# Kernel optimization log

Measured on AMD Instinct MI355X. Metric: run time of the kernel, lower is better.

## Reference

```python
import jax, jax.numpy as jnp
import numpy as np

B, S, HID = 1, 2048, 2048
NH, NKV = 32, 8
HD = HID // NH  # 64
WINDOW = 1024
ROPE_BASE = 500000.0


def setup_inputs() -> dict:
    key = jax.random.key(0)
    ks = jax.random.split(key, 5)
    sc = 0.02
    return {
        "hidden_states": jax.random.normal(ks[0], (B, S, HID), dtype=jnp.float32),
        "Wq": jax.random.normal(ks[1], (HID, NH * HD), dtype=jnp.float32) * sc,
        "Wk": jax.random.normal(ks[2], (HID, NKV * HD), dtype=jnp.float32) * sc,
        "Wv": jax.random.normal(ks[3], (HID, NKV * HD), dtype=jnp.float32) * sc,
        "Wo": jax.random.normal(ks[4], (NH * HD, HID), dtype=jnp.float32) * sc,
    }


def _rope_cos_sin(seq_len, dtype):
    inv_freq = 1.0 / (ROPE_BASE ** (jnp.arange(0, HD, 2, dtype=jnp.float32) / HD))
    pos = jnp.arange(seq_len, dtype=jnp.float32)
    freqs = pos[:, None] * inv_freq[None, :]          # [S, HD/2]
    emb = jnp.concatenate([freqs, freqs], axis=-1)    # [S, HD]
    return jnp.cos(emb).astype(dtype), jnp.sin(emb).astype(dtype)


def _rotate_half(x):
    x1, x2 = x[..., : HD // 2], x[..., HD // 2:]
    return jnp.concatenate([-x2, x1], axis=-1)


def reference(hidden_states, Wq, Wk, Wv, Wo):
    b, s, _ = hidden_states.shape
    q = (hidden_states @ Wq).reshape(b, s, NH, HD).transpose(0, 2, 1, 3)   # [B,NH,S,D]
    k = (hidden_states @ Wk).reshape(b, s, NKV, HD).transpose(0, 2, 1, 3)  # [B,NKV,S,D]
    v = (hidden_states @ Wv).reshape(b, s, NKV, HD).transpose(0, 2, 1, 3)

    cos, sin = _rope_cos_sin(s, hidden_states.dtype)  # [S, D]
    cos, sin = cos[None, None], sin[None, None]       # [1,1,S,D]
    q = q * cos + _rotate_half(q) * sin
    k = k * cos + _rotate_half(k) * sin

    n_rep = NH // NKV
    k = jnp.repeat(k, n_rep, axis=1)  # [B,NH,S,D]
    v = jnp.repeat(v, n_rep, axis=1)

    # sliding-window causal additive mask
    row = jnp.arange(s)[:, None]
    col = jnp.arange(s)[None, :]
    banned = (col > row) | (col < row - WINDOW + 1)
    mask = jnp.where(banned, jnp.float32(-jnp.inf), 0.0).astype(hidden_states.dtype)

    scale = 1.0 / np.sqrt(HD)
    scores = jnp.einsum("bhqd,bhkd->bhqk", q, k) * scale + mask
    attn = jax.nn.softmax(scores, axis=-1)
    out = jnp.einsum("bhqk,bhkd->bhqd", attn, v)          # [B,NH,S,D]
    out = out.transpose(0, 2, 1, 3).reshape(b, s, NH * HD)
    return out @ Wo
```

## Files before the change

kernel.cpp:

```cpp
#include <hip/hip_runtime.h>
#include <hip/hip_bf16.h>
#include <math.h>

#define S_LEN 2048
#define HID 2048
#define NH 32
#define NKV 8
#define HD 64
#define WINDOW 1024
#define QBLK 128
#define QKVN 3072

typedef __attribute__((ext_vector_type(8))) short bx8;
typedef __attribute__((ext_vector_type(4))) float fx4;
typedef __attribute__((ext_vector_type(8))) unsigned short us8;

#define GL_LDS16(gp, lp) \
    __builtin_amdgcn_global_load_lds((__attribute__((address_space(1))) const void*)(gp), \
                                     (__attribute__((address_space(3))) void*)(lp), 16, 0, 0)

__global__ __launch_bounds__(256) void prep_kernel(const float* __restrict__ hs,
                                                   const float* __restrict__ Wq,
                                                   const float* __restrict__ Wk,
                                                   const float* __restrict__ Wv,
                                                   const float* __restrict__ Wo,
                                                   float* __restrict__ cosT, float* __restrict__ sinT,
                                                   __hip_bfloat16* __restrict__ hsb,
                                                   __hip_bfloat16* __restrict__ WqkvT,
                                                   __hip_bfloat16* __restrict__ WoT) {
    __shared__ float tile[32][33];
    int b = blockIdx.x, t = threadIdx.x;
    if (b < 256) {
        int idx = b * 256 + t;
        int s = idx >> 5, f = idx & 31;
        double inv = exp(-2.0 * (double)f / 64.0 * log(500000.0));
        double ang = (double)s * inv;
        cosT[idx] = (float)cos(ang);
        sinT[idx] = (float)sin(ang);
        return;
    }
    b -= 256;
    if (b < 2048) {
        int i = (b * 256 + t) * 8;
        float4 a = *reinterpret_cast<const float4*>(&hs[i]);
        float4 c = *reinterpret_cast<const float4*>(&hs[i + 4]);
        __hip_bfloat16 o[8] __attribute__((aligned(16)));
        o[0] = __float2bfloat16(a.x); o[1] = __float2bfloat16(a.y);
        o[2] = __float2bfloat16(a.z); o[3] = __float2bfloat16(a.w);
        o[4] = __float2bfloat16(c.x); o[5] = __float2bfloat16(c.y);
        o[6] = __float2bfloat16(c.z); o[7] = __float2bfloat16(c.w);
        *reinterpret_cast<bx8*>(&hsb[i]) = *reinterpret_cast<bx8*>(o);
        return;
    }
    b -= 2048;
    const float* src; __hip_bfloat16* dst; int Nd, bx, by;
    if (b < 4096)      { src = Wq; dst = WqkvT;                        Nd = 2048; bx = b & 63; by = b >> 6; }
    else if (b < 5120) { b -= 4096; src = Wk; dst = WqkvT + (size_t)2048 * 2048; Nd = 512; bx = b & 15; by = b >> 4; }
    else if (b < 6144) { b -= 5120; src = Wv; dst = WqkvT + (size_t)2560 * 2048; Nd = 512; bx = b & 15; by = b >> 4; }
    else               { b -= 6144; src = Wo; dst = WoT;               Nd = 2048; bx = b & 63; by = b >> 6; }
    int n0 = bx * 32, k0 = by * 32, tx = t & 31, ty = t >> 5;
#pragma unroll
    for (int i = 0; i < 4; i++)
        tile[ty + 8 * i][tx] = src[(size_t)(k0 + ty + 8 * i) * Nd + n0 + tx];
    __syncthreads();
#pragma unroll
    for (int i = 0; i < 4; i++)
        dst[(size_t)(n0 + ty + 8 * i) * 2048 + k0 + tx] = __float2bfloat16(tile[tx][ty + 8 * i]);
}

__global__ __launch_bounds__(256) void ropev_kernel(__hip_bfloat16* __restrict__ QKV,
                                                    __hip_bfloat16* __restrict__ Vt,
                                                    const float* __restrict__ cosT,
                                                    const float* __restrict__ sinT) {
    __shared__ __hip_bfloat16 tile[32][33];
    int b = blockIdx.x, t = threadIdx.x;
    if (b < 10240) {
        int idx = b * 256 + t;
        int f = idx & 31;
        int head = (idx >> 5) % (NH + NKV);
        int s = idx / ((NH + NKV) * 32);
        float c  = cosT[(s << 5) + f];
        float sn = sinT[(s << 5) + f];
        __hip_bfloat16* p = (head < NH) ? (QKV + (size_t)s * QKVN + head * HD)
                                        : (QKV + (size_t)s * QKVN + 2048 + (head - NH) * HD);
        float x1 = __bfloat162float(p[f]), x2 = __bfloat162float(p[f + 32]);
        p[f]      = __float2bfloat16(x1 * c - x2 * sn);
        p[f + 32] = __float2bfloat16(x2 * c + x1 * sn);
        return;
    }
    b -= 10240;
    int s0 = (b & 63) * 32, d0 = (b >> 6) * 32;
    int tx = t & 31, ty = t >> 5;
#pragma unroll
    for (int i = 0; i < 4; i++)
        tile[ty + 8 * i][tx] = QKV[(size_t)(s0 + ty + 8 * i) * QKVN + 2560 + d0 + tx];
    __syncthreads();
#pragma unroll
    for (int i = 0; i < 4; i++)
        Vt[(size_t)(d0 + ty + 8 * i) * S_LEN + s0 + tx] = tile[tx][ty + 8 * i];
}

template <int OUTBF16>
__global__ __launch_bounds__(256) void gemm_pipe_kernel(const __hip_bfloat16* __restrict__ A,
                                                        const __hip_bfloat16* __restrict__ Bt,
                                                        void* __restrict__ Cp,
                                                        int M, int N, int K, int stripe) {
    __shared__ __hip_bfloat16 As[3][2048];
    __shared__ __hip_bfloat16 Bs[3][4096];

    const int bid = blockIdx.x;
    const int x = bid & 7, j = bid >> 3;
    const int bn = (x * stripe + j % stripe) * 128;
    const int bm = (j / stripe) * 64;

    const int t = threadIdx.x, w = t >> 6, l = t & 63;
    const int wr = (w >> 1) * 32, wc = (w & 1) * 64;
    const int lr = l & 15;
    const int rdslot = (((l >> 4) ^ ((lr >> 1) & 3))) * 8;
    const int srow = w * 16 + (l >> 2);
    const int scol = (((l & 3) ^ ((l >> 3) & 3))) * 8;
    const int ldsoff = w * 512;

    const __hip_bfloat16* ga0 = A + (size_t)(bm + srow) * K + scol;
    const __hip_bfloat16* gb0 = Bt + (size_t)(bn + srow) * K + scol;
    const size_t half = (size_t)64 * K;

    fx4 acc[2][4];
#pragma unroll
    for (int m = 0; m < 2; m++)
#pragma unroll
        for (int n = 0; n < 4; n++) acc[m][n] = (fx4){0.f, 0.f, 0.f, 0.f};

    const int T = K >> 5;

#define STAGE(kt, b)                                              \
    do {                                                          \
        const __hip_bfloat16* ga = ga0 + (kt) * 32;               \
        const __hip_bfloat16* gb = gb0 + (kt) * 32;               \
        GL_LDS16(ga,        &As[(b)][ldsoff]);                    \
        GL_LDS16(gb,        &Bs[(b)][ldsoff]);                    \
        GL_LDS16(gb + half, &Bs[(b)][2048 + ldsoff]);             \
    } while (0)

    STAGE(0, 0);
    STAGE(1, 1);

    for (int i = 0; i < T; i++) {
        const int r = i % 3;
        if (i + 1 < T) asm volatile("s_waitcnt vmcnt(3)" ::: "memory");
        else           asm volatile("s_waitcnt vmcnt(0)" ::: "memory");
        __builtin_amdgcn_s_barrier();
        asm volatile("" ::: "memory");
        if (i + 2 < T) STAGE(i + 2, (i + 2) % 3);

        bx8 af[2], bf[4];
#pragma unroll
        for (int m = 0; m < 2; m++)
            af[m] = *reinterpret_cast<const bx8*>(&As[r][(wr + m * 16 + lr) * 32 + rdslot]);
#pragma unroll
        for (int n = 0; n < 4; n++)
            bf[n] = *reinterpret_cast<const bx8*>(&Bs[r][(wc + n * 16 + lr) * 32 + rdslot]);
#pragma unroll
        for (int m = 0; m < 2; m++)
#pragma unroll
            for (int n = 0; n < 4; n++)
                acc[m][n] = __builtin_amdgcn_mfma_f32_16x16x32_bf16(af[m], bf[n], acc[m][n], 0, 0, 0);
    }
#undef STAGE

    const int lq = (l >> 4) * 4;
#pragma unroll
    for (int m = 0; m < 2; m++)
#pragma unroll
        for (int n = 0; n < 4; n++)
#pragma unroll
            for (int r2 = 0; r2 < 4; r2++) {
                int row = bm + wr + m * 16 + lq + r2;
                int col = bn + wc + n * 16 + lr;
                float v = acc[m][n][r2];
                if (OUTBF16)
                    ((__hip_bfloat16*)Cp)[(size_t)row * N + col] = __float2bfloat16(v);
                else
                    ((float*)Cp)[(size_t)row * N + col] = v;
            }
}

__global__ __launch_bounds__(512, 4) void attn_kernel(const __hip_bfloat16* __restrict__ Q,
                                                      const __hip_bfloat16* __restrict__ Kg,
                                                      const __hip_bfloat16* __restrict__ Vtg,
                                                      __hip_bfloat16* __restrict__ Ab) {
    __shared__ __hip_bfloat16 Ks[64 * 64];
    __shared__ __hip_bfloat16 Vs[64 * 64];
    __shared__ __hip_bfloat16 Ps[QBLK * 64];

    const int bid = blockIdx.x;
    const int swz = (bid & 7) * 64 + (bid >> 3);
    const int h = swz >> 4, qi = swz & 15;
    const int qb = qi * QBLK;
    const int kvh = h >> 2;

    const int t = threadIdx.x, w = t >> 6, l = t & 63;
    const int lr = l & 15, g = l >> 4, lk = g * 8;
    const int qbw = qb + 16 * w;
    const int prow = 16 * w + lr;
    const int psz = (prow & 7) << 4;

    char* KsB = (char*)Ks;
    char* VsB = (char*)Vs;
    char* PsB = (char*)Ps;

    bx8 qa[2];
#pragma unroll
    for (int ks = 0; ks < 2; ks++)
        qa[ks] = *reinterpret_cast<const bx8*>(
            &Q[(size_t)(qbw + lr) * QKVN + h * HD + ks * 32 + lk]);

    fx4 ot[4];
#pragma unroll
    for (int n = 0; n < 4; n++) ot[n] = (fx4){0.f, 0.f, 0.f, 0.f};
    float mrow = -1e30f, srow = 0.f;

    const int k0_first = (qb >= 1024) ? (qb - 1024) : 0;
    const int k0_last  = qb + 64;
    const int wmax = qbw + 15;
    const int rowq = qbw + lr;

    const int sr = t >> 3, sc8 = (t & 7) * 8;
    const int dst = sr * 128 + ((sc8 * 2) ^ ((sr & 7) << 4));

    for (int k0 = k0_first; k0 <= k0_last; k0 += 64) {
        us8 kv = *reinterpret_cast<const us8*>(&Kg[(size_t)(k0 + sr) * QKVN + kvh * HD + sc8]);
        us8 vv = *reinterpret_cast<const us8*>(&Vtg[(size_t)(kvh * HD + sr) * S_LEN + k0 + sc8]);
        *reinterpret_cast<us8*>(KsB + dst) = kv;
        *reinterpret_cast<us8*>(VsB + dst) = vv;
        __syncthreads();

        if (k0 <= wmax) {
            bx8 kb[4][2];
#pragma unroll
            for (int n = 0; n < 4; n++)
#pragma unroll
                for (int ks = 0; ks < 2; ks++) {
                    int row = 16 * n + lr;
                    kb[n][ks] = *reinterpret_cast<const bx8*>(
                        KsB + row * 128 + (((ks * 64) + 16 * g) ^ ((row & 7) << 4)));
                }
            fx4 sc[4];
#pragma unroll
            for (int n = 0; n < 4; n++) {
                sc[n] = __builtin_amdgcn_mfma_f32_16x16x32_bf16(kb[n][0], qa[0],
                                                                (fx4){0.f, 0.f, 0.f, 0.f}, 0, 0, 0);
                sc[n] = __builtin_amdgcn_mfma_f32_16x16x32_bf16(kb[n][1], qa[1], sc[n], 0, 0, 0);
            }
            const bool interior = (k0 + 63 <= qbw) && (k0 >= qbw - 1008);
            if (interior) {
#pragma unroll
                for (int n = 0; n < 4; n++)
#pragma unroll
                    for (int r = 0; r < 4; r++) sc[n][r] *= 0.125f;
            } else {
#pragma unroll
                for (int n = 0; n < 4; n++)
#pragma unroll
                    for (int r = 0; r < 4; r++) {
                        int key = k0 + 16 * n + 4 * g + r;
                        bool valid = (key <= rowq) && (key >= rowq - (WINDOW - 1));
                        sc[n][r] = valid ? sc[n][r] * 0.125f : -1e30f;
                    }
            }
            float tmax = fmaxf(fmaxf(sc[0][0], sc[0][1]), fmaxf(sc[0][2], sc[0][3]));
#pragma unroll
            for (int n = 1; n < 4; n++)
                tmax = fmaxf(tmax, fmaxf(fmaxf(sc[n][0], sc[n][1]), fmaxf(sc[n][2], sc[n][3])));
            tmax = fmaxf(tmax, __shfl_xor(tmax, 16));
            tmax = fmaxf(tmax, __shfl_xor(tmax, 32));
            float mn = fmaxf(mrow, tmax);
            float fs = __expf(mrow - mn);
            mrow = mn;
            float ps = 0.f;
#pragma unroll
            for (int n = 0; n < 4; n++) {
#pragma unroll
                for (int r = 0; r < 4; r++) {
                    float p = __expf(sc[n][r] - mn);
                    sc[n][r] = p;
                    ps += p;
                }
                __hip_bfloat16 pk[4] __attribute__((aligned(8)));
                pk[0] = __float2bfloat16(sc[n][0]); pk[1] = __float2bfloat16(sc[n][1]);
                pk[2] = __float2bfloat16(sc[n][2]); pk[3] = __float2bfloat16(sc[n][3]);
                *reinterpret_cast<unsigned long long*>(PsB + prow * 128 + ((32 * n + 8 * g) ^ psz)) =
                    *reinterpret_cast<unsigned long long*>(pk);
            }
            ps += __shfl_xor(ps, 16);
            ps += __shfl_xor(ps, 32);
            srow = srow * fs + ps;
#pragma unroll
            for (int n = 0; n < 4; n++)
#pragma unroll
                for (int r = 0; r < 4; r++) ot[n][r] *= fs;
            bx8 vb[4][2];
#pragma unroll
            for (int n = 0; n < 4; n++)
#pragma unroll
                for (int ks = 0; ks < 2; ks++) {
                    int row = 16 * n + lr;
                    vb[n][ks] = *reinterpret_cast<const bx8*>(
                        VsB + row * 128 + (((ks * 64) + 16 * g) ^ ((row & 7) << 4)));
                }
            bx8 pb[2];
#pragma unroll
            for (int ks = 0; ks < 2; ks++)
                pb[ks] = *reinterpret_cast<const bx8*>(
                    PsB + prow * 128 + (((ks * 64) + 16 * g) ^ psz));
#pragma unroll
            for (int n = 0; n < 4; n++) {
                ot[n] = __builtin_amdgcn_mfma_f32_16x16x32_bf16(vb[n][0], pb[0], ot[n], 0, 0, 0);
                ot[n] = __builtin_amdgcn_mfma_f32_16x16x32_bf16(vb[n][1], pb[1], ot[n], 0, 0, 0);
            }
        }
        __syncthreads();
    }

    const float inv = 1.f / srow;
#pragma unroll
    for (int n = 0; n < 4; n++) {
        __hip_bfloat16 pk[4] __attribute__((aligned(8)));
#pragma unroll
        for (int r = 0; r < 4; r++) pk[r] = __float2bfloat16(ot[n][r] * inv);
        *reinterpret_cast<unsigned long long*>(PsB + prow * 128 + ((32 * n + 8 * g) ^ psz)) =
            *reinterpret_cast<unsigned long long*>(pk);
    }
    __syncthreads();
#pragma unroll
    for (int j = 0; j < 2; j++) {
        const int row = (t >> 3) + 64 * j, c = t & 7;
        us8 v = *reinterpret_cast<const us8*>(PsB + row * 128 + ((c * 16) ^ ((row & 7) << 4)));
        *reinterpret_cast<us8*>(&Ab[(size_t)(qb + row) * HID + h * HD + c * 8]) = v;
    }
}

extern "C" void kernel_launch(void* const* d_in, const int* in_sizes, int n_in,
                              void* d_out, int out_size, void* d_ws, size_t ws_size,
                              hipStream_t stream) {
    const float* hs = (const float*)d_in[0];
    const float* Wq = (const float*)d_in[1];
    const float* Wk = (const float*)d_in[2];
    const float* Wv = (const float*)d_in[3];
    const float* Wo = (const float*)d_in[4];

    float* ws   = (float*)d_ws;
    float* cosT = ws;
    float* sinT = cosT + 65536;
    __hip_bfloat16* hsb    = (__hip_bfloat16*)(sinT + 65536);
    __hip_bfloat16* WqkvT  = hsb + 4194304;
    __hip_bfloat16* WoT    = WqkvT + 6291456;
    __hip_bfloat16* QKVb   = WoT + 4194304;
    __hip_bfloat16* Vt     = QKVb + 6291456;
    __hip_bfloat16* Ab     = hsb;

    prep_kernel<<<12544, 256, 0, stream>>>(hs, Wq, Wk, Wv, Wo, cosT, sinT, hsb, WqkvT, WoT);

    gemm_pipe_kernel<1><<<768, 256, 0, stream>>>(hsb, WqkvT, QKVb, 2048, QKVN, 2048, 3);

    ropev_kernel<<<11264, 256, 0, stream>>>(QKVb, Vt, cosT, sinT);

    attn_kernel<<<512, 512, 0, stream>>>(QKVb, QKVb + 2048, Vt, Ab);

    gemm_pipe_kernel<0><<<512, 256, 0, stream>>>(Ab, WoT, d_out, 2048, 2048, 2048, 2);
}
```

Measured before the change: 144.7 us.

## Double-buffer K/V tiles in attention via direct global-to-LDS async loads

The attention kernel now keeps two LDS buffers each for K and V and prefetches the next 64-key tile with global_load_lds while the current tile is processed. Register-staged loads with swizzled LDS stores are replaced by direct 16-byte global-to-LDS copies, with the swizzle moved to the global source address. The loop uses a single waitcnt+barrier per iteration instead of two syncthreads. This is meant to hide K/V load latency behind the MFMA/softmax work, at the cost of doubled K/V LDS and reliance on the per-wave LDS layout of global_load_lds matching the swizzled read pattern.

```diff
diff --git a/kernel.cpp b/kernel.cpp
--- a/kernel.cpp
+++ b/kernel.cpp
@@ -189,8 +189,8 @@
                                                       const __hip_bfloat16* __restrict__ Kg,
                                                       const __hip_bfloat16* __restrict__ Vtg,
                                                       __hip_bfloat16* __restrict__ Ab) {
-    __shared__ __hip_bfloat16 Ks[64 * 64];
-    __shared__ __hip_bfloat16 Vs[64 * 64];
+    __shared__ __hip_bfloat16 Ks[2][4096];
+    __shared__ __hip_bfloat16 Vs[2][4096];
     __shared__ __hip_bfloat16 Ps[QBLK * 64];
 
     const int bid = blockIdx.x;
@@ -205,8 +205,6 @@
     const int prow = 16 * w + lr;
     const int psz = (prow & 7) << 4;
 
-    char* KsB = (char*)Ks;
-    char* VsB = (char*)Vs;
     char* PsB = (char*)Ps;
 
     bx8 qa[2];
@@ -225,17 +223,32 @@
     const int wmax = qbw + 15;
     const int rowq = qbw + lr;
 
-    const int sr = t >> 3, sc8 = (t & 7) * 8;
-    const int dst = sr * 128 + ((sc8 * 2) ^ ((sr & 7) << 4));
-
-    for (int k0 = k0_first; k0 <= k0_last; k0 += 64) {
-        us8 kv = *reinterpret_cast<const us8*>(&Kg[(size_t)(k0 + sr) * QKVN + kvh * HD + sc8]);
-        us8 vv = *reinterpret_cast<const us8*>(&Vtg[(size_t)(kvh * HD + sr) * S_LEN + k0 + sc8]);
-        *reinterpret_cast<us8*>(KsB + dst) = kv;
-        *reinterpret_cast<us8*>(VsB + dst) = vv;
-        __syncthreads();
+    const int sr = t >> 3, c8 = t & 7;
+    const int scolsw = 8 * (c8 ^ (sr & 7));
+    const int kcol = kvh * HD + scolsw;
+    const int vrow = kvh * HD + sr;
+    __hip_bfloat16* ldsK = &Ks[0][0] + (t >> 6) * 512;
+    __hip_bfloat16* ldsV = &Vs[0][0] + (t >> 6) * 512;
+
+#define ASTAGE(k0v, p)                                                           \
+    do {                                                                         \
+        GL_LDS16(&Kg[(size_t)((k0v) + sr) * QKVN + kcol], ldsK + (p) * 4096);    \
+        GL_LDS16(&Vtg[(size_t)vrow * S_LEN + (k0v) + scolsw], ldsV + (p) * 4096);\
+    } while (0)
+
+    ASTAGE(k0_first, 0);
+
+    int ti = 0;
+    for (int k0 = k0_first; k0 <= k0_last; k0 += 64, ++ti) {
+        const int p = ti & 1;
+        asm volatile("s_waitcnt vmcnt(0)" ::: "memory");
+        __builtin_amdgcn_s_barrier();
+        asm volatile("" ::: "memory");
+        if (k0 + 64 <= k0_last) ASTAGE(k0 + 64, p ^ 1);
 
         if (k0 <= wmax) {
+            char* KsB = (char*)&Ks[p][0];
+            char* VsB = (char*)&Vs[p][0];
             bx8 kb[4][2];
 #pragma unroll
             for (int n = 0; n < 4; n++)
@@ -282,9 +295,9 @@
             for (int n = 0; n < 4; n++) {
 #pragma unroll
                 for (int r = 0; r < 4; r++) {
-                    float p = __expf(sc[n][r] - mn);
-                    sc[n][r] = p;
-                    ps += p;
+                    float p2 = __expf(sc[n][r] - mn);
+                    sc[n][r] = p2;
+                    ps += p2;
                 }
                 __hip_bfloat16 pk[4] __attribute__((aligned(8)));
                 pk[0] = __float2bfloat16(sc[n][0]); pk[1] = __float2bfloat16(sc[n][1]);
@@ -319,8 +332,8 @@
                 ot[n] = __builtin_amdgcn_mfma_f32_16x16x32_bf16(vb[n][1], pb[1], ot[n], 0, 0, 0);
             }
         }
-        __syncthreads();
-    }
+    }
+#undef ASTAGE
 
     const float inv = 1.f / srow;
 #pragma unroll
```

New measurement: 144.7 us. About the same (+0.0%).
